# Kernel optimization log

Hardware: AMD Instinct MI355X
Metric: run time of the kernel (lower is better)

Reference implementation:

```python
import jax, jax.numpy as jnp
import numpy as np

N_NODES = 50000
N_EDGES = 800000
HID = 128
EDGE_FEAT = 4
NUM_G = 20
R_MIN, R_MAX = 0.0, 100.0  # r_max = 10.0**2


def _mlp2(x, w1, b1, w2, b2, act_last):
    y = jax.nn.relu(x @ w1 + b1)
    y = y @ w2 + b2
    return jax.nn.relu(y) if act_last else y


def _linear_init(key, fan_in, fan_out):
    kw, kb = jax.random.split(key)
    lim = 1.0 / np.sqrt(fan_in)
    w = jax.random.uniform(kw, (fan_in, fan_out), jnp.float32, -lim, lim)
    b = jax.random.uniform(kb, (fan_out,), jnp.float32, -lim, lim)
    return w, b


def setup_inputs():
    key = jax.random.key(0)
    ks = jax.random.split(key, 16)
    src = jax.random.randint(ks[0], (N_EDGES,), 0, N_NODES)
    dst = jax.random.randint(ks[1], (N_EDGES,), 0, N_NODES)
    edge_feat = jax.random.normal(ks[2], (N_EDGES, EDGE_FEAT), jnp.float32)
    h = jax.random.normal(ks[3], (N_NODES, HID), jnp.float32)
    x = jax.random.normal(ks[4], (N_NODES, 3), jnp.float32)
    ein = 2 * HID + EDGE_FEAT + NUM_G
    ew1, eb1 = _linear_init(ks[5], ein, HID)
    ew2, eb2 = _linear_init(ks[6], HID, HID)
    infw, infb = _linear_init(ks[7], HID, 1)
    xw1, xb1 = _linear_init(ks[8], HID, HID)
    xw2, xb2 = _linear_init(ks[9], HID, 1)
    nw1, nb1 = _linear_init(ks[10], 2 * HID, HID)
    nw2, nb2 = _linear_init(ks[11], HID, HID)
    return {"src": src, "dst": dst, "edge_feat": edge_feat, "h": h, "x": x,
            "ew1": ew1, "eb1": eb1, "ew2": ew2, "eb2": eb2,
            "infw": infw, "infb": infb,
            "xw1": xw1, "xb1": xb1, "xw2": xw2, "xb2": xb2,
            "nw1": nw1, "nb1": nb1, "nw2": nw2, "nb2": nb2}


def reference(src, dst, edge_feat, h, x,
              ew1, eb1, ew2, eb2, infw, infb,
              xw1, xb1, xw2, xb2, nw1, nb1, nw2, nb2):
    n_nodes = h.shape[0]
    rel_x = x[dst] - x[src]                      # [E, 3]
    r = jnp.sum(rel_x * rel_x, -1, keepdims=True)  # [E, 1]
    # GaussianSmearing expansion
    offsets = jnp.linspace(R_MIN, R_MAX, NUM_G)
    coeff = -0.5 / (offsets[1] - offsets[0]) ** 2
    r_feat = jnp.exp(coeff * (r - offsets) ** 2)  # [E, NUM_G]
    # edge message MLP (act_last=True)
    cat = jnp.concatenate([edge_feat, r_feat, h[dst], h[src]], axis=-1)
    mij = _mlp2(cat, ew1, eb1, ew2, eb2, act_last=True)  # [E, HID]
    eij = jax.nn.sigmoid(mij @ infw + infb)              # [E, 1]
    mi = jax.ops.segment_sum(mij * eij, dst, num_segments=n_nodes)  # [N, HID]
    h_new = h + _mlp2(jnp.concatenate([mi, h], -1), nw1, nb1, nw2, nb2, act_last=False)
    # coordinate update: (xi - xj) == rel_x
    x_scale = _mlp2(mij, xw1, xb1, xw2, xb2, act_last=False)  # [E, 1]
    delta_x = jax.ops.segment_sum(rel_x * x_scale, dst, num_segments=n_nodes)
    x_new = x + delta_x
    return h_new, x_new
```

## Files before the change

kernel.cpp:

```cpp
#include <hip/hip_runtime.h>

#define HID 128
#define NNODES 50000
#define NEDGES 800000

typedef __attribute__((ext_vector_type(8))) short short8;
typedef __attribute__((ext_vector_type(4))) float f32x4;

union U8 { short8 v; unsigned short u[8]; };

__device__ __forceinline__ unsigned short f2b(float f) {
  unsigned int u = __float_as_uint(f);
  u += 0x7FFFu + ((u >> 16) & 1u);
  return (unsigned short)(u >> 16);
}

__device__ __forceinline__ void atomicPkAddBf16(unsigned short* addr, unsigned int packed) {
  asm volatile("global_atomic_pk_add_bf16 %0, %1, off" :: "v"(addr), "v"(packed) : "memory");
}

__global__ __launch_bounds__(256) void pack_kernel(
    const float* __restrict__ ew1, const float* __restrict__ ew2,
    const float* __restrict__ xw1, const float* __restrict__ nw1,
    const float* __restrict__ nw2, unsigned short* __restrict__ ws) {
  int i = blockIdx.x * 256 + threadIdx.x;
  const float* w; int base, ksrc;
  if (i < 36864)       { w = ew1; base = 0;      ksrc = 280; }
  else if (i < 53248)  { w = ew2; base = 36864;  ksrc = 128; }
  else if (i < 69632)  { w = xw1; base = 53248;  ksrc = 128; }
  else if (i < 102400) { w = nw1; base = 69632;  ksrc = 256; }
  else if (i < 118784) { w = nw2; base = 102400; ksrc = 128; }
  else return;
  int li = i - base;
  int j = li & 7, t = li >> 3;
  int col = t & 127, kg = t >> 7;
  int k = kg * 8 + j;
  float v = (k < ksrc) ? w[k * 128 + col] : 0.0f;
  ws[i] = f2b(v);
}

template<int MIBF16>
__global__ __launch_bounds__(256, 4) void edge_kernel(
    const int* __restrict__ src, const int* __restrict__ dst,
    const float* __restrict__ ef, const float* __restrict__ h,
    const float* __restrict__ x,
    const float* __restrict__ eb1, const float* __restrict__ eb2,
    const float* __restrict__ infw, const float* __restrict__ infb,
    const float* __restrict__ xb1, const float* __restrict__ xw2,
    const float* __restrict__ xb2,
    const short8* __restrict__ W1p, const short8* __restrict__ W2p,
    const short8* __restrict__ XW1p,
    float* __restrict__ miF, unsigned short* __restrict__ miB,
    float* __restrict__ dx) {
  __shared__ __align__(16) char catB[64 * 576];
  __shared__ int dL[64], sL[64];
  __shared__ float relL[64][3];
  __shared__ float ppart[4][64];
  __shared__ float eijL[64];

  const int tid = threadIdx.x;
  const int e0 = blockIdx.x * 64;

  if (tid < 64) {
    int e = e0 + tid;
    int s = src[e], d = dst[e];
    sL[tid] = s; dL[tid] = d;
    float rx = x[3*d+0] - x[3*s+0];
    float ry = x[3*d+1] - x[3*s+1];
    float rz = x[3*d+2] - x[3*s+2];
    relL[tid][0] = rx; relL[tid][1] = ry; relL[tid][2] = rz;
    float r = rx*rx + ry*ry + rz*rz;
    float vals[24];
    const float4 efv = reinterpret_cast<const float4*>(ef)[e];
    vals[0]=efv.x; vals[1]=efv.y; vals[2]=efv.z; vals[3]=efv.w;
    const float step = 100.0f / 19.0f;
    const float co = -0.5f / (step * step);
    #pragma unroll
    for (int g = 0; g < 20; ++g) {
      float t = r - (float)g * step;
      vals[4+g] = __expf(co * t * t);
    }
    #pragma unroll
    for (int c = 0; c < 3; ++c) {
      U8 u;
      #pragma unroll
      for (int j = 0; j < 8; ++j) u.u[j] = f2b(vals[c*8+j]);
      *reinterpret_cast<short8*>(catB + tid*576 + ((c ^ (tid&7))<<4)) = u.v;
    }
    U8 z;
    #pragma unroll
    for (int j = 0; j < 8; ++j) z.u[j] = 0;
    *reinterpret_cast<short8*>(catB + tid*576 + ((32 + (3 ^ (tid&3)))<<4)) = z.v;
  }
  __syncthreads();

  for (int i = tid; i < 64*32; i += 256) {
    int row = i >> 5, c = i & 31;
    int node = (c < 16) ? dL[row] : sL[row];
    const float4* hp = reinterpret_cast<const float4*>(h + node*128 + (c&15)*8);
    float4 a = hp[0], b = hp[1];
    U8 u;
    u.u[0]=f2b(a.x); u.u[1]=f2b(a.y); u.u[2]=f2b(a.z); u.u[3]=f2b(a.w);
    u.u[4]=f2b(b.x); u.u[5]=f2b(b.y); u.u[6]=f2b(b.z); u.u[7]=f2b(b.w);
    int chunk = 3 + c;
    int sw = (chunk < 32) ? (chunk ^ (row&7)) : (32 + ((chunk&3) ^ (row&3)));
    *reinterpret_cast<short8*>(catB + row*576 + (sw<<4)) = u.v;
  }
  __syncthreads();

  const int lane = tid & 63, w = tid >> 6;
  const int lr = lane & 15, lg = lane >> 4;
  const int l7 = lr & 7, l3 = lr & 3;
  const int colb = w*32 + lr;

  f32x4 acc[4][2];
  #pragma unroll
  for (int t = 0; t < 4; ++t) { acc[t][0] = (f32x4)0.0f; acc[t][1] = (f32x4)0.0f; }
  #pragma unroll
  for (int kt = 0; kt < 9; ++kt) {
    int ch = (kt < 8) ? ((kt*4+lg) ^ l7) : (32 + (lg ^ l3));
    short8 a0 = *reinterpret_cast<const short8*>(catB + (0*16+lr)*576 + (ch<<4));
    short8 a1 = *reinterpret_cast<const short8*>(catB + (1*16+lr)*576 + (ch<<4));
    short8 a2 = *reinterpret_cast<const short8*>(catB + (2*16+lr)*576 + (ch<<4));
    short8 a3 = *reinterpret_cast<const short8*>(catB + (3*16+lr)*576 + (ch<<4));
    short8 b0 = W1p[(kt*4+lg)*128 + colb];
    short8 b1 = W1p[(kt*4+lg)*128 + colb + 16];
    acc[0][0] = __builtin_amdgcn_mfma_f32_16x16x32_bf16(a0, b0, acc[0][0], 0, 0, 0);
    acc[0][1] = __builtin_amdgcn_mfma_f32_16x16x32_bf16(a0, b1, acc[0][1], 0, 0, 0);
    acc[1][0] = __builtin_amdgcn_mfma_f32_16x16x32_bf16(a1, b0, acc[1][0], 0, 0, 0);
    acc[1][1] = __builtin_amdgcn_mfma_f32_16x16x32_bf16(a1, b1, acc[1][1], 0, 0, 0);
    acc[2][0] = __builtin_amdgcn_mfma_f32_16x16x32_bf16(a2, b0, acc[2][0], 0, 0, 0);
    acc[2][1] = __builtin_amdgcn_mfma_f32_16x16x32_bf16(a2, b1, acc[2][1], 0, 0, 0);
    acc[3][0] = __builtin_amdgcn_mfma_f32_16x16x32_bf16(a3, b0, acc[3][0], 0, 0, 0);
    acc[3][1] = __builtin_amdgcn_mfma_f32_16x16x32_bf16(a3, b1, acc[3][1], 0, 0, 0);
  }
  __syncthreads();

  {
    float be0 = eb1[colb], be1 = eb1[colb+16];
    #pragma unroll
    for (int t = 0; t < 4; ++t)
      #pragma unroll
      for (int j = 0; j < 2; ++j) {
        float bias = j ? be1 : be0;
        int col = w*32 + j*16 + lr;
        #pragma unroll
        for (int rg = 0; rg < 4; ++rg) {
          int row = t*16 + lg*4 + rg;
          float v = fmaxf(acc[t][j][rg] + bias, 0.f);
          int chunk = (col>>3) ^ (row&7);
          *reinterpret_cast<unsigned short*>(catB + row*576 + (chunk<<4) + ((col&7)<<1)) = f2b(v);
        }
      }
  }
  __syncthreads();

  f32x4 acc2[4][2];
  #pragma unroll
  for (int t = 0; t < 4; ++t) { acc2[t][0] = (f32x4)0.0f; acc2[t][1] = (f32x4)0.0f; }
  #pragma unroll
  for (int kt = 0; kt < 4; ++kt) {
    int ch = (kt*4+lg) ^ l7;
    short8 a0 = *reinterpret_cast<const short8*>(catB + (0*16+lr)*576 + (ch<<4));
    short8 a1 = *reinterpret_cast<const short8*>(catB + (1*16+lr)*576 + (ch<<4));
    short8 a2 = *reinterpret_cast<const short8*>(catB + (2*16+lr)*576 + (ch<<4));
    short8 a3 = *reinterpret_cast<const short8*>(catB + (3*16+lr)*576 + (ch<<4));
    short8 b0 = W2p[(kt*4+lg)*128 + colb];
    short8 b1 = W2p[(kt*4+lg)*128 + colb + 16];
    acc2[0][0] = __builtin_amdgcn_mfma_f32_16x16x32_bf16(a0, b0, acc2[0][0], 0, 0, 0);
    acc2[0][1] = __builtin_amdgcn_mfma_f32_16x16x32_bf16(a0, b1, acc2[0][1], 0, 0, 0);
    acc2[1][0] = __builtin_amdgcn_mfma_f32_16x16x32_bf16(a1, b0, acc2[1][0], 0, 0, 0);
    acc2[1][1] = __builtin_amdgcn_mfma_f32_16x16x32_bf16(a1, b1, acc2[1][1], 0, 0, 0);
    acc2[2][0] = __builtin_amdgcn_mfma_f32_16x16x32_bf16(a2, b0, acc2[2][0], 0, 0, 0);
    acc2[2][1] = __builtin_amdgcn_mfma_f32_16x16x32_bf16(a2, b1, acc2[2][1], 0, 0, 0);
    acc2[3][0] = __builtin_amdgcn_mfma_f32_16x16x32_bf16(a3, b0, acc2[3][0], 0, 0, 0);
    acc2[3][1] = __builtin_amdgcn_mfma_f32_16x16x32_bf16(a3, b1, acc2[3][1], 0, 0, 0);
  }
  {
    float be0 = eb2[colb], be1 = eb2[colb+16];
    float iw0 = infw[colb], iw1 = infw[colb+16];
    float pl[4][4];
    #pragma unroll
    for (int t = 0; t < 4; ++t)
      #pragma unroll
      for (int rg = 0; rg < 4; ++rg) pl[t][rg] = 0.f;
    #pragma unroll
    for (int t = 0; t < 4; ++t)
      #pragma unroll
      for (int j = 0; j < 2; ++j) {
        float bias = j ? be1 : be0;
        float iw = j ? iw1 : iw0;
        int col = w*32 + j*16 + lr;
        #pragma unroll
        for (int rg = 0; rg < 4; ++rg) {
          int row = t*16 + lg*4 + rg;
          float v = fmaxf(acc2[t][j][rg] + bias, 0.f);
          acc2[t][j][rg] = v;
          pl[t][rg] += v * iw;
          int chunk = 16 + (((col>>3)&15) ^ (row&7));
          *reinterpret_cast<unsigned short*>(catB + row*576 + (chunk<<4) + ((col&7)<<1)) = f2b(v);
        }
      }
    #pragma unroll
    for (int m = 1; m < 16; m <<= 1)
      #pragma unroll
      for (int t = 0; t < 4; ++t)
        #pragma unroll
        for (int rg = 0; rg < 4; ++rg) pl[t][rg] += __shfl_xor(pl[t][rg], m, 64);
    if (lr == 0) {
      #pragma unroll
      for (int t = 0; t < 4; ++t)
        #pragma unroll
        for (int rg = 0; rg < 4; ++rg) ppart[w][t*16 + lg*4 + rg] = pl[t][rg];
    }
  }
  __syncthreads();

  if (tid < 64) {
    float s = ppart[0][tid] + ppart[1][tid] + ppart[2][tid] + ppart[3][tid] + infb[0];
    eijL[tid] = 1.f / (1.f + __expf(-s));
  }
  __syncthreads();

  #pragma unroll
  for (int t = 0; t < 4; ++t)
    #pragma unroll
    for (int rg = 0; rg < 4; ++rg) {
      int row = t*16 + lg*4 + rg;
      int d = dL[row];
      float e = eijL[row];
      float u0 = acc2[t][0][rg] * e;
      float u1 = acc2[t][1][rg] * e;
      if (MIBF16) {
        float got = __shfl_xor((lr & 1) ? u0 : u1, 1, 64);
        int col0; unsigned short lo, hi;
        if (!(lr & 1)) { col0 = w*32 + lr;          lo = f2b(u0);  hi = f2b(got); }
        else           { col0 = w*32 + 16 + lr - 1; lo = f2b(got); hi = f2b(u1); }
        unsigned int packed = (unsigned int)lo | ((unsigned int)hi << 16);
        atomicPkAddBf16(miB + d*128 + col0, packed);
      } else {
        atomicAdd(miF + d*128 + colb,      u0);
        atomicAdd(miF + d*128 + colb + 16, u1);
      }
    }

  f32x4 acc3[4][2];
  #pragma unroll
  for (int t = 0; t < 4; ++t) { acc3[t][0] = (f32x4)0.0f; acc3[t][1] = (f32x4)0.0f; }
  #pragma unroll
  for (int kt = 0; kt < 4; ++kt) {
    int ch = 16 + ((kt*4+lg) ^ l7);
    short8 a0 = *reinterpret_cast<const short8*>(catB + (0*16+lr)*576 + (ch<<4));
    short8 a1 = *reinterpret_cast<const short8*>(catB + (1*16+lr)*576 + (ch<<4));
    short8 a2 = *reinterpret_cast<const short8*>(catB + (2*16+lr)*576 + (ch<<4));
    short8 a3 = *reinterpret_cast<const short8*>(catB + (3*16+lr)*576 + (ch<<4));
    short8 b0 = XW1p[(kt*4+lg)*128 + colb];
    short8 b1 = XW1p[(kt*4+lg)*128 + colb + 16];
    acc3[0][0] = __builtin_amdgcn_mfma_f32_16x16x32_bf16(a0, b0, acc3[0][0], 0, 0, 0);
    acc3[0][1] = __builtin_amdgcn_mfma_f32_16x16x32_bf16(a0, b1, acc3[0][1], 0, 0, 0);
    acc3[1][0] = __builtin_amdgcn_mfma_f32_16x16x32_bf16(a1, b0, acc3[1][0], 0, 0, 0);
    acc3[1][1] = __builtin_amdgcn_mfma_f32_16x16x32_bf16(a1, b1, acc3[1][1], 0, 0, 0);
    acc3[2][0] = __builtin_amdgcn_mfma_f32_16x16x32_bf16(a2, b0, acc3[2][0], 0, 0, 0);
    acc3[2][1] = __builtin_amdgcn_mfma_f32_16x16x32_bf16(a2, b1, acc3[2][1], 0, 0, 0);
    acc3[3][0] = __builtin_amdgcn_mfma_f32_16x16x32_bf16(a3, b0, acc3[3][0], 0, 0, 0);
    acc3[3][1] = __builtin_amdgcn_mfma_f32_16x16x32_bf16(a3, b1, acc3[3][1], 0, 0, 0);
  }
  {
    float bx0 = xb1[colb], bx1 = xb1[colb+16];
    float xwv0 = xw2[colb], xwv1 = xw2[colb+16];
    float ql[4][4];
    #pragma unroll
    for (int t = 0; t < 4; ++t)
      #pragma unroll
      for (int rg = 0; rg < 4; ++rg) ql[t][rg] = 0.f;
    #pragma unroll
    for (int t = 0; t < 4; ++t)
      #pragma unroll
      for (int j = 0; j < 2; ++j) {
        float bias = j ? bx1 : bx0;
        float xwv = j ? xwv1 : xwv0;
        #pragma unroll
        for (int rg = 0; rg < 4; ++rg) {
          float v = fmaxf(acc3[t][j][rg] + bias, 0.f);
          ql[t][rg] += v * xwv;
        }
      }
    #pragma unroll
    for (int m = 1; m < 16; m <<= 1)
      #pragma unroll
      for (int t = 0; t < 4; ++t)
        #pragma unroll
        for (int rg = 0; rg < 4; ++rg) ql[t][rg] += __shfl_xor(ql[t][rg], m, 64);
    if (lr == 0) {
      #pragma unroll
      for (int t = 0; t < 4; ++t)
        #pragma unroll
        for (int rg = 0; rg < 4; ++rg) ppart[w][t*16 + lg*4 + rg] = ql[t][rg];
    }
  }
  __syncthreads();

  if (tid < 192) {
    int row = tid / 3, c = tid - row*3;
    float q = ppart[0][row] + ppart[1][row] + ppart[2][row] + ppart[3][row] + xb2[0];
    atomicAdd(dx + dL[row]*3 + c, relL[row][c] * q);
  }
}

template<int MIBF16>
__global__ __launch_bounds__(256) void node_kernel(
    const float* __restrict__ h, const float* __restrict__ x,
    const float* __restrict__ nb1, const float* __restrict__ nb2,
    const short8* __restrict__ NW1p, const short8* __restrict__ NW2p,
    const unsigned short* __restrict__ miB,
    float* __restrict__ out) {
  __shared__ __align__(16) char c2B[64 * 512];
  __shared__ __align__(16) char y3B[64 * 256];
  const int tid = threadIdx.x;
  const int n0 = blockIdx.x * 64;
  const float* mi = out;

  for (int i = tid; i < 64*32; i += 256) {
    int row = i >> 5, c = i & 31;
    int node = n0 + row;
    U8 u;
    if (node < NNODES) {
      if (c < 16 && MIBF16) {
        u.v = *reinterpret_cast<const short8*>(miB + node*128 + c*8);
      } else {
        const float4* p = (c < 16)
          ? reinterpret_cast<const float4*>(mi + node*128 + c*8)
          : reinterpret_cast<const float4*>(h + node*128 + (c-16)*8);
        float4 a = p[0], b = p[1];
        u.u[0]=f2b(a.x); u.u[1]=f2b(a.y); u.u[2]=f2b(a.z); u.u[3]=f2b(a.w);
        u.u[4]=f2b(b.x); u.u[5]=f2b(b.y); u.u[6]=f2b(b.z); u.u[7]=f2b(b.w);
      }
    } else {
      #pragma unroll
      for (int j = 0; j < 8; ++j) u.u[j] = 0;
    }
    *reinterpret_cast<short8*>(c2B + row*512 + ((c ^ (row&7))<<4)) = u.v;
  }
  __syncthreads();

  const int lane = tid & 63, wave = tid >> 6;
  const int lr = lane & 15, lg = lane >> 4;
  const int rb = wave * 16;
  const int arow = rb + lr;

  f32x4 acc[8];
  #pragma unroll
  for (int nt = 0; nt < 8; ++nt) acc[nt] = (f32x4)0.0f;
  #pragma unroll
  for (int kt = 0; kt < 8; ++kt) {
    int chunk = kt*4 + lg;
    short8 a = *reinterpret_cast<const short8*>(c2B + arow*512 + ((chunk ^ (arow&7))<<4));
    const short8* bp = NW1p + chunk*128 + lr;
    #pragma unroll
    for (int nt = 0; nt < 8; ++nt)
      acc[nt] = __builtin_amdgcn_mfma_f32_16x16x32_bf16(a, bp[nt*16], acc[nt], 0, 0, 0);
  }
  #pragma unroll
  for (int nt = 0; nt < 8; ++nt) {
    int col = nt*16 + lr;
    float bias = nb1[col];
    #pragma unroll
    for (int r = 0; r < 4; ++r) {
      int row = rb + lg*4 + r;
      float v = fmaxf(acc[nt][r] + bias, 0.f);
      *reinterpret_cast<unsigned short*>(y3B + row*256 + (((col>>3) ^ (row&7))<<4) + ((col&7)<<1)) = f2b(v);
    }
  }

  f32x4 acc2[8];
  #pragma unroll
  for (int nt = 0; nt < 8; ++nt) acc2[nt] = (f32x4)0.0f;
  #pragma unroll
  for (int kt = 0; kt < 4; ++kt) {
    int chunk = kt*4 + lg;
    short8 a = *reinterpret_cast<const short8*>(y3B + arow*256 + ((chunk ^ (arow&7))<<4));
    const short8* bp = NW2p + chunk*128 + lr;
    #pragma unroll
    for (int nt = 0; nt < 8; ++nt)
      acc2[nt] = __builtin_amdgcn_mfma_f32_16x16x32_bf16(a, bp[nt*16], acc2[nt], 0, 0, 0);
  }
  __syncthreads();
  #pragma unroll
  for (int nt = 0; nt < 8; ++nt) {
    int col = nt*16 + lr;
    float b2 = nb2[col];
    #pragma unroll
    for (int r = 0; r < 4; ++r) {
      int row = rb + lg*4 + r;
      int node = n0 + row;
      if (node < NNODES) {
        int idx = node*128 + col;
        out[idx] = acc2[nt][r] + b2 + h[idx];
      }
    }
  }

  if (tid < 192) {
    int node = n0 + tid/3;
    if (node < NNODES) {
      int idx = node*3 + (tid%3);
      float* xo = out + NNODES*HID;
      xo[idx] = x[idx] + xo[idx];
    }
  }
}

extern "C" void kernel_launch(void* const* d_in, const int* in_sizes, int n_in,
                              void* d_out, int out_size, void* d_ws, size_t ws_size,
                              hipStream_t stream) {
  const int*   src  = (const int*)  d_in[0];
  const int*   dst  = (const int*)  d_in[1];
  const float* ef   = (const float*)d_in[2];
  const float* h    = (const float*)d_in[3];
  const float* x    = (const float*)d_in[4];
  const float* ew1  = (const float*)d_in[5];
  const float* eb1  = (const float*)d_in[6];
  const float* ew2  = (const float*)d_in[7];
  const float* eb2  = (const float*)d_in[8];
  const float* infw = (const float*)d_in[9];
  const float* infb = (const float*)d_in[10];
  const float* xw1  = (const float*)d_in[11];
  const float* xb1  = (const float*)d_in[12];
  const float* xw2  = (const float*)d_in[13];
  const float* xb2  = (const float*)d_in[14];
  const float* nw1  = (const float*)d_in[15];
  const float* nb1  = (const float*)d_in[16];
  const float* nw2  = (const float*)d_in[17];
  const float* nb2  = (const float*)d_in[18];

  float* out = (float*)d_out;
  float* miF = out;
  float* dxp = out + NNODES*HID;
  unsigned short* wsp = (unsigned short*)d_ws;
  unsigned short* miB = wsp + 118784;

  size_t need = 118784u*2u + (size_t)NNODES*HID*2u;
  int mib = (ws_size >= need) ? 1 : 0;

  if (mib) {
    hipMemsetAsync(miB, 0, (size_t)NNODES*HID*2, stream);
    hipMemsetAsync(dxp, 0, (size_t)NNODES*3*4, stream);
  } else {
    hipMemsetAsync(d_out, 0, (size_t)out_size * sizeof(float), stream);
  }

  pack_kernel<<<464, 256, 0, stream>>>(ew1, ew2, xw1, nw1, nw2, wsp);

  if (mib) {
    edge_kernel<1><<<NEDGES/64, 256, 0, stream>>>(
        src, dst, ef, h, x, eb1, eb2, infw, infb, xb1, xw2, xb2,
        (const short8*)wsp, (const short8*)(wsp + 36864), (const short8*)(wsp + 53248),
        miF, miB, dxp);
    node_kernel<1><<<(NNODES + 63)/64, 256, 0, stream>>>(
        h, x, nb1, nb2,
        (const short8*)(wsp + 69632), (const short8*)(wsp + 102400), miB, out);
  } else {
    edge_kernel<0><<<NEDGES/64, 256, 0, stream>>>(
        src, dst, ef, h, x, eb1, eb2, infw, infb, xb1, xw2, xb2,
        (const short8*)wsp, (const short8*)(wsp + 36864), (const short8*)(wsp + 53248),
        miF, miB, dxp);
    node_kernel<0><<<(NNODES + 63)/64, 256, 0, stream>>>(
        h, x, nb1, nb2,
        (const short8*)(wsp + 69632), (const short8*)(wsp + 102400), miB, out);
  }
}
```

Measured before the change: 354.1 us.

## Parallelize edge prologue across all threads, pack bf16 pairs, prefetch W1

```diff
diff --git a/kernel.cpp b/kernel.cpp
--- a/kernel.cpp
+++ b/kernel.cpp
@@ -13,6 +13,14 @@
   unsigned int u = __float_as_uint(f);
   u += 0x7FFFu + ((u >> 16) & 1u);
   return (unsigned short)(u >> 16);
+}
+
+__device__ __forceinline__ unsigned int pk2(float a, float b) {
+  unsigned int ua = __float_as_uint(a);
+  ua += 0x7FFFu + ((ua >> 16) & 1u);
+  unsigned int ub = __float_as_uint(b);
+  ub += 0x7FFFu + ((ub >> 16) & 1u);
+  return (ua >> 16) | (ub & 0xFFFF0000u);
 }
 
 __device__ __forceinline__ void atomicPkAddBf16(unsigned short* addr, unsigned int packed) {
@@ -60,58 +68,70 @@
 
   const int tid = threadIdx.x;
   const int e0 = blockIdx.x * 64;
-
-  if (tid < 64) {
-    int e = e0 + tid;
-    int s = src[e], d = dst[e];
-    sL[tid] = s; dL[tid] = d;
-    float rx = x[3*d+0] - x[3*s+0];
-    float ry = x[3*d+1] - x[3*s+1];
-    float rz = x[3*d+2] - x[3*s+2];
-    relL[tid][0] = rx; relL[tid][1] = ry; relL[tid][2] = rz;
-    float r = rx*rx + ry*ry + rz*rz;
-    float vals[24];
-    const float4 efv = reinterpret_cast<const float4*>(ef)[e];
-    vals[0]=efv.x; vals[1]=efv.y; vals[2]=efv.z; vals[3]=efv.w;
-    const float step = 100.0f / 19.0f;
-    const float co = -0.5f / (step * step);
-    #pragma unroll
-    for (int g = 0; g < 20; ++g) {
-      float t = r - (float)g * step;
-      vals[4+g] = __expf(co * t * t);
-    }
-    #pragma unroll
-    for (int c = 0; c < 3; ++c) {
-      U8 u;
-      #pragma unroll
-      for (int j = 0; j < 8; ++j) u.u[j] = f2b(vals[c*8+j]);
-      *reinterpret_cast<short8*>(catB + tid*576 + ((c ^ (tid&7))<<4)) = u.v;
-    }
-    U8 z;
-    #pragma unroll
-    for (int j = 0; j < 8; ++j) z.u[j] = 0;
-    *reinterpret_cast<short8*>(catB + tid*576 + ((32 + (3 ^ (tid&3)))<<4)) = z.v;
-  }
-  __syncthreads();
-
-  for (int i = tid; i < 64*32; i += 256) {
-    int row = i >> 5, c = i & 31;
-    int node = (c < 16) ? dL[row] : sL[row];
-    const float4* hp = reinterpret_cast<const float4*>(h + node*128 + (c&15)*8);
-    float4 a = hp[0], b = hp[1];
-    U8 u;
-    u.u[0]=f2b(a.x); u.u[1]=f2b(a.y); u.u[2]=f2b(a.z); u.u[3]=f2b(a.w);
-    u.u[4]=f2b(b.x); u.u[5]=f2b(b.y); u.u[6]=f2b(b.z); u.u[7]=f2b(b.w);
-    int chunk = 3 + c;
-    int sw = (chunk < 32) ? (chunk ^ (row&7)) : (32 + ((chunk&3) ^ (row&3)));
-    *reinterpret_cast<short8*>(catB + row*576 + (sw<<4)) = u.v;
-  }
-  __syncthreads();
-
   const int lane = tid & 63, w = tid >> 6;
   const int lr = lane & 15, lg = lane >> 4;
   const int l7 = lr & 7, l3 = lr & 3;
   const int colb = w*32 + lr;
+
+  {
+    int row = tid >> 2, sub = tid & 3;
+    int e = e0 + row;
+    int s = src[e], d = dst[e];
+    if (sub == 0) { sL[row] = s; dL[row] = d; }
+    float rx = x[3*d+0] - x[3*s+0];
+    float ry = x[3*d+1] - x[3*s+1];
+    float rz = x[3*d+2] - x[3*s+2];
+    if (sub == 1) { relL[row][0] = rx; relL[row][1] = ry; relL[row][2] = rz; }
+    float r = rx*rx + ry*ry + rz*rz;
+    const float step = 100.0f / 19.0f;
+    const float co = -0.5f / (step * step);
+    float v6[6];
+    if (sub == 0) {
+      const float4 efv = reinterpret_cast<const float4*>(ef)[e];
+      v6[0]=efv.x; v6[1]=efv.y; v6[2]=efv.z; v6[3]=efv.w;
+      float t1 = r - step;
+      v6[4] = __expf(co * r * r);
+      v6[5] = __expf(co * t1 * t1);
+    } else {
+      #pragma unroll
+      for (int q = 0; q < 6; ++q) {
+        float g = (float)(sub*6 - 4 + q) * step;
+        float t = r - g;
+        v6[q] = __expf(co * t * t);
+      }
+    }
+    #pragma unroll
+    for (int q = 0; q < 3; ++q) {
+      int c = sub*6 + q*2;
+      int chunk = (c>>3) ^ (row&7);
+      *reinterpret_cast<unsigned int*>(catB + row*576 + (chunk<<4) + ((c&7)<<1)) = pk2(v6[q*2], v6[q*2+1]);
+    }
+    if (sub == 3) {
+      U8 z;
+      #pragma unroll
+      for (int j = 0; j < 8; ++j) z.u[j] = 0;
+      *reinterpret_cast<short8*>(catB + row*576 + ((32 + (3 ^ (row&3)))<<4)) = z.v;
+    }
+  }
+
+  #pragma unroll
+  for (int it = 0; it < 8; ++it) {
+    int i = tid + it*256;
+    int row = i >> 5, c = i & 31;
+    int node = (c < 16) ? dst[e0+row] : src[e0+row];
+    const float4* hp = reinterpret_cast<const float4*>(h + node*128 + (c&15)*8);
+    float4 a = hp[0], b = hp[1];
+    uint4 u;
+    u.x = pk2(a.x, a.y); u.y = pk2(a.z, a.w);
+    u.z = pk2(b.x, b.y); u.w = pk2(b.z, b.w);
+    int chunk = 3 + c;
+    int sw = (chunk < 32) ? (chunk ^ (row&7)) : (32 + ((chunk&3) ^ (row&3)));
+    *reinterpret_cast<uint4*>(catB + row*576 + (sw<<4)) = u;
+  }
+
+  short8 p00 = W1p[(0*4+lg)*128 + colb], p01 = W1p[(0*4+lg)*128 + colb + 16];
+  short8 p10 = W1p[(1*4+lg)*128 + colb], p11 = W1p[(1*4+lg)*128 + colb + 16];
+  __syncthreads();
 
   f32x4 acc[4][2];
   #pragma unroll
@@ -123,8 +143,10 @@
     short8 a1 = *reinterpret_cast<const short8*>(catB + (1*16+lr)*576 + (ch<<4));
     short8 a2 = *reinterpret_cast<const short8*>(catB + (2*16+lr)*576 + (ch<<4));
     short8 a3 = *reinterpret_cast<const short8*>(catB + (3*16+lr)*576 + (ch<<4));
-    short8 b0 = W1p[(kt*4+lg)*128 + colb];
-    short8 b1 = W1p[(kt*4+lg)*128 + colb + 16];
+    short8 b0, b1;
+    if (kt == 0)      { b0 = p00; b1 = p01; }
+    else if (kt == 1) { b0 = p10; b1 = p11; }
+    else              { b0 = W1p[(kt*4+lg)*128 + colb]; b1 = W1p[(kt*4+lg)*128 + colb + 16]; }
     acc[0][0] = __builtin_amdgcn_mfma_f32_16x16x32_bf16(a0, b0, acc[0][0], 0, 0, 0);
     acc[0][1] = __builtin_amdgcn_mfma_f32_16x16x32_bf16(a0, b1, acc[0][1], 0, 0, 0);
     acc[1][0] = __builtin_amdgcn_mfma_f32_16x16x32_bf16(a1, b0, acc[1][0], 0, 0, 0);
@@ -141,16 +163,17 @@
     #pragma unroll
     for (int t = 0; t < 4; ++t)
       #pragma unroll
-      for (int j = 0; j < 2; ++j) {
-        float bias = j ? be1 : be0;
-        int col = w*32 + j*16 + lr;
-        #pragma unroll
-        for (int rg = 0; rg < 4; ++rg) {
-          int row = t*16 + lg*4 + rg;
-          float v = fmaxf(acc[t][j][rg] + bias, 0.f);
-          int chunk = (col>>3) ^ (row&7);
-          *reinterpret_cast<unsigned short*>(catB + row*576 + (chunk<<4) + ((col&7)<<1)) = f2b(v);
-        }
+      for (int rg = 0; rg < 4; ++rg) {
+        int row = t*16 + lg*4 + rg;
+        float v0 = fmaxf(acc[t][0][rg] + be0, 0.f);
+        float v1 = fmaxf(acc[t][1][rg] + be1, 0.f);
+        float send = (lr & 1) ? v0 : v1;
+        float got = __shfl_xor(send, 1, 64);
+        int col0; unsigned int pv;
+        if (!(lr & 1)) { col0 = w*32 + lr;          pv = pk2(v0, got); }
+        else           { col0 = w*32 + 16 + lr - 1; pv = pk2(got, v1); }
+        int chunk = (col0>>3) ^ (row&7);
+        *reinterpret_cast<unsigned int*>(catB + row*576 + (chunk<<4) + ((col0&7)<<1)) = pv;
       }
   }
   __syncthreads();
@@ -187,19 +210,19 @@
     #pragma unroll
     for (int t = 0; t < 4; ++t)
       #pragma unroll
-      for (int j = 0; j < 2; ++j) {
-        float bias = j ? be1 : be0;
-        float iw = j ? iw1 : iw0;
-        int col = w*32 + j*16 + lr;
-        #pragma unroll
-        for (int rg = 0; rg < 4; ++rg) {
-          int row = t*16 + lg*4 + rg;
-          float v = fmaxf(acc2[t][j][rg] + bias, 0.f);
-          acc2[t][j][rg] = v;
-          pl[t][rg] += v * iw;
-          int chunk = 16 + (((col>>3)&15) ^ (row&7));
-          *reinterpret_cast<unsigned short*>(catB + row*576 + (chunk<<4) + ((col&7)<<1)) = f2b(v);
-        }
+      for (int rg = 0; rg < 4; ++rg) {
+        int row = t*16 + lg*4 + rg;
+        float v0 = fmaxf(acc2[t][0][rg] + be0, 0.f);
+        float v1 = fmaxf(acc2[t][1][rg] + be1, 0.f);
+        acc2[t][0][rg] = v0; acc2[t][1][rg] = v1;
+        pl[t][rg] += v0*iw0 + v1*iw1;
+        float send = (lr & 1) ? v0 : v1;
+        float got = __shfl_xor(send, 1, 64);
+        int col0; unsigned int pv;
+        if (!(lr & 1)) { col0 = w*32 + lr;          pv = pk2(v0, got); }
+        else           { col0 = w*32 + 16 + lr - 1; pv = pk2(got, v1); }
+        int chunk = 16 + (((col0>>3)&15) ^ (row&7));
+        *reinterpret_cast<unsigned int*>(catB + row*576 + (chunk<<4) + ((col0&7)<<1)) = pv;
       }
     #pragma unroll
     for (int m = 1; m < 16; m <<= 1)
@@ -216,9 +239,10 @@
   }
   __syncthreads();
 
-  if (tid < 64) {
-    float s = ppart[0][tid] + ppart[1][tid] + ppart[2][tid] + ppart[3][tid] + infb[0];
-    eijL[tid] = 1.f / (1.f + __expf(-s));
+  if (lane < 16) {
+    int row2 = w*16 + lane;
+    float s2 = ppart[0][row2] + ppart[1][row2] + ppart[2][row2] + ppart[3][row2] + infb[0];
+    eijL[row2] = 1.f / (1.f + __expf(-s2));
   }
   __syncthreads();
 
@@ -233,10 +257,9 @@
       float u1 = acc2[t][1][rg] * e;
       if (MIBF16) {
         float got = __shfl_xor((lr & 1) ? u0 : u1, 1, 64);
-        int col0; unsigned short lo, hi;
-        if (!(lr & 1)) { col0 = w*32 + lr;          lo = f2b(u0);  hi = f2b(got); }
-        else           { col0 = w*32 + 16 + lr - 1; lo = f2b(got); hi = f2b(u1); }
-        unsigned int packed = (unsigned int)lo | ((unsigned int)hi << 16);
+        int col0; unsigned int packed;
+        if (!(lr & 1)) { col0 = w*32 + lr;          packed = pk2(u0, got); }
+        else           { col0 = w*32 + 16 + lr - 1; packed = pk2(got, u1); }
         atomicPkAddBf16(miB + d*128 + col0, packed);
       } else {
         atomicAdd(miF + d*128 + colb,      u0);
@@ -276,14 +299,10 @@
     #pragma unroll
     for (int t = 0; t < 4; ++t)
       #pragma unroll
-      for (int j = 0; j < 2; ++j) {
-        float bias = j ? bx1 : bx0;
-        float xwv = j ? xwv1 : xwv0;
-        #pragma unroll
-        for (int rg = 0; rg < 4; ++rg) {
-          float v = fmaxf(acc3[t][j][rg] + bias, 0.f);
-          ql[t][rg] += v * xwv;
-        }
+      for (int rg = 0; rg < 4; ++rg) {
+        float v0 = fmaxf(acc3[t][0][rg] + bx0, 0.f);
+        float v1 = fmaxf(acc3[t][1][rg] + bx1, 0.f);
+        ql[t][rg] += v0*xwv0 + v1*xwv1;
       }
     #pragma unroll
     for (int m = 1; m < 16; m <<= 1)
@@ -332,8 +351,10 @@
           ? reinterpret_cast<const float4*>(mi + node*128 + c*8)
           : reinterpret_cast<const float4*>(h + node*128 + (c-16)*8);
         float4 a = p[0], b = p[1];
-        u.u[0]=f2b(a.x); u.u[1]=f2b(a.y); u.u[2]=f2b(a.z); u.u[3]=f2b(a.w);
-        u.u[4]=f2b(b.x); u.u[5]=f2b(b.y); u.u[6]=f2b(b.z); u.u[7]=f2b(b.w);
+        uint4 uu;
+        uu.x = pk2(a.x, a.y); uu.y = pk2(a.z, a.w);
+        uu.z = pk2(b.x, b.y); uu.w = pk2(b.z, b.w);
+        u.v = *reinterpret_cast<short8*>(&uu);
       }
     } else {
       #pragma unroll
```

Result: slower. 370.2 us (+4.5%).
